# Optimization experiments

Hardware: AMD Instinct MI355X
Metric: run time of the kernel (lower is better)

Reference implementation:

```python
import jax, jax.numpy as jnp
import numpy as np

B, C, N, T, H = 4, 128, 512, 16, 4
DK = C // H
SCALE = float(np.sqrt(DK) * 1.0)  # dk**0.5 * max(tau,1e-6), tau=1.0


def setup_inputs() -> dict:
    key = jax.random.key(0)
    ks = jax.random.split(key, 6)
    x = jax.random.normal(ks[0], (B, C, N, T), jnp.float32)
    Wq = jax.random.normal(ks[1], (C, C), jnp.float32) * (1.0 / np.sqrt(C))
    Wk = jax.random.normal(ks[2], (C, C), jnp.float32) * (1.0 / np.sqrt(C))
    # original init is identity; add tiny noise so it's not degenerate
    structural = jnp.eye(N, dtype=jnp.float32) + 0.01 * jax.random.normal(ks[3], (N, N), jnp.float32)
    fusion_w = jax.random.normal(ks[4], (2,), jnp.float32) * 0.5  # 1x1 conv over 2 input channels
    fusion_b = (jax.random.normal(ks[5], (), jnp.float32) * 0.1)
    return {"x": x, "Wq": Wq, "Wk": Wk, "structural": structural,
            "fusion_w": fusion_w, "fusion_b": fusion_b}


def reference(x, Wq, Wk, structural, fusion_w, fusion_b):
    # x: [B, C, N, T]. 1x1 conv == per-channel linear; arrange to [B,T,N,H,DK]
    Q = jnp.einsum('oc,bcnt->btno', Wq, x).reshape(B, T, N, H, DK)
    K = jnp.einsum('oc,bcnt->btno', Wk, x).reshape(B, T, N, H, DK)
    # scores: [B, T, H, N, N]
    scores = jnp.einsum('btnhd,btmhd->bthnm', Q, K) / SCALE
    att_node = jax.nn.softmax(scores, axis=-1).mean(axis=(1, 2))  # [B, N, N]
    att_struct = jax.nn.softmax(structural, axis=-1)              # [N, N]
    # fusion conv (1x1, 2->1 channels) == weighted sum + bias
    fused = fusion_w[0] * att_node + fusion_w[1] * att_struct[None] + fusion_b
    fused = 0.5 * (fused + jnp.swapaxes(fused, 1, 2))  # symmetrize
    fused = jax.nn.softmax(fused, axis=-1)             # normalize='softmax'
    x_bt = jnp.transpose(x, (0, 3, 2, 1))              # [B, T, N, C]
    x_att = jnp.einsum('bij,btjc->btic', fused, x_bt)  # weighted aggregation over nodes
    return jnp.transpose(x_att, (0, 3, 2, 1))          # [B, C, N, T]
```

## Files before the change

kernel.cpp:

```cpp
#include <hip/hip_runtime.h>

#define BB 4
#define CC 128
#define NN 512
#define TT 16
#define HH 4
#define DKK 32
#define INV_SCALE 0.17677669529663687f

typedef __attribute__((ext_vector_type(8))) short bf16x8;
typedef __attribute__((ext_vector_type(4))) float f32x4;

__device__ __forceinline__ unsigned int pk2bf(float a, float b) {
  unsigned int ua = __float_as_uint(a);
  ua = (ua + 0x7FFFu + ((ua >> 16) & 1u)) >> 16;
  unsigned int ub = __float_as_uint(b);
  ub = (ub + 0x7FFFu + ((ub >> 16) & 1u)) >> 16;
  return ua | (ub << 16);
}

__device__ __forceinline__ ushort cv1(float f) {
  unsigned int u = __float_as_uint(f);
  return (ushort)((u + 0x7FFFu + ((u >> 16) & 1u)) >> 16);
}

__device__ __forceinline__ unsigned int pkfast(float a, float b) {
  unsigned int au = __float_as_uint(a) + 0x8000u;
  unsigned int bu = __float_as_uint(b) + 0x8000u;
  return __builtin_amdgcn_perm(bu, au, 0x07060302u);
}

__global__ __launch_bounds__(256) void k_wconv(const float* __restrict__ Wq,
                                               const float* __restrict__ Wk,
                                               ushort* __restrict__ Wqb,
                                               ushort* __restrict__ Wkb) {
  const int gid = blockIdx.x * 256 + threadIdx.x;
  const int i = gid * 4;
  const float* src = (i < 16384) ? (Wq + i) : (Wk + i - 16384);
  ushort* dst = (i < 16384) ? (Wqb + i) : (Wkb + i - 16384);
  float4 v = *(const float4*)src;
  uint2 u;
  u.x = pk2bf(v.x, v.y);
  u.y = pk2bf(v.z, v.w);
  *(uint2*)dst = u;
}

__global__ __launch_bounds__(256) void k_proj(const float* __restrict__ x,
                                              const ushort* __restrict__ Wqb,
                                              const ushort* __restrict__ Wkb,
                                              ushort* __restrict__ Qb,
                                              ushort* __restrict__ Kb) {
  __shared__ float xl[128 * 128];
  const int b = blockIdx.y;
  const int nt0 = blockIdx.x * 128;
  const int tid = threadIdx.x;
  const int w = tid >> 6, lane = tid & 63;
  const int lm = lane & 15, quad = lane >> 4;

  const float* xb = x + (size_t)b * 1048576 + nt0;
#pragma unroll
  for (int L = tid * 4; L < 16384; L += 1024) {
    int c = L >> 7, j = L & 127;
    *(float4*)(xl + L) = *(const float4*)(xb + c * 8192 + j);
  }

  const int o0 = w * 32;
  bf16x8 aq[2][4], ak[2][4];
#pragma unroll
  for (int ot = 0; ot < 2; ++ot)
#pragma unroll
    for (int kc = 0; kc < 4; ++kc) {
      int off = (o0 + ot * 16 + lm) * 128 + kc * 32 + quad * 8;
      aq[ot][kc] = *(const bf16x8*)(Wqb + off);
      ak[ot][kc] = *(const bf16x8*)(Wkb + off);
    }
  __syncthreads();

  const int nq = nt0 >> 4;
#pragma unroll 2
  for (int jt = 0; jt < 8; ++jt) {
    bf16x8 bfr[4];
#pragma unroll
    for (int kc = 0; kc < 4; ++kc) {
      const float* sp = xl + (kc * 32 + quad * 8) * 128 + jt * 16 + lm;
      float f0 = sp[0],   f1 = sp[128], f2 = sp[256], f3 = sp[384];
      float f4 = sp[512], f5 = sp[640], f6 = sp[768], f7 = sp[896];
      uint4 u;
      u.x = pkfast(f0, f1);
      u.y = pkfast(f2, f3);
      u.z = pkfast(f4, f5);
      u.w = pkfast(f6, f7);
      union { uint4 u; bf16x8 v; } cv;
      cv.u = u;
      bfr[kc] = cv.v;
    }

    f32x4 accq0 = {0,0,0,0}, accq1 = {0,0,0,0};
    f32x4 acck0 = {0,0,0,0}, acck1 = {0,0,0,0};
#pragma unroll
    for (int kc = 0; kc < 4; ++kc) {
      accq0 = __builtin_amdgcn_mfma_f32_16x16x32_bf16(aq[0][kc], bfr[kc], accq0, 0, 0, 0);
      accq1 = __builtin_amdgcn_mfma_f32_16x16x32_bf16(aq[1][kc], bfr[kc], accq1, 0, 0, 0);
      acck0 = __builtin_amdgcn_mfma_f32_16x16x32_bf16(ak[0][kc], bfr[kc], acck0, 0, 0, 0);
      acck1 = __builtin_amdgcn_mfma_f32_16x16x32_bf16(ak[1][kc], bfr[kc], acck1, 0, 0, 0);
    }

    const size_t base = (size_t)b * 1048576 + (size_t)lm * 65536 + w * 16384 +
                        (size_t)(nq + jt) * 32 + quad * 4;
    uint2 uq0, uq1, uk0, uk1;
    uq0.x = pk2bf(accq0[0], accq0[1]); uq0.y = pk2bf(accq0[2], accq0[3]);
    uq1.x = pk2bf(accq1[0], accq1[1]); uq1.y = pk2bf(accq1[2], accq1[3]);
    uk0.x = pk2bf(acck0[0], acck0[1]); uk0.y = pk2bf(acck0[2], acck0[3]);
    uk1.x = pk2bf(acck1[0], acck1[1]); uk1.y = pk2bf(acck1[2], acck1[3]);
    *(uint2*)(Qb + base)      = uq0;
    *(uint2*)(Qb + base + 16) = uq1;
    *(uint2*)(Kb + base)      = uk0;
    *(uint2*)(Kb + base + 16) = uk1;
  }
}

__global__ __launch_bounds__(64) void k_scores(const ushort* __restrict__ Qb,
                                               const ushort* __restrict__ Kb,
                                               ushort* __restrict__ part) {
  __shared__ float SH[16 * 516];
  const int strip = blockIdx.x, g = blockIdx.y, b = blockIdx.z;
  const int lane = threadIdx.x;
  const int lm = lane & 15, quad = lane >> 4;
  const int n0 = strip * 16;
  const int d0 = quad * 8;
  const int r2 = lane >> 2, cb2 = (lane & 3) * 4;
  const int rsel = r2 & 3;

  float acc[128];
#pragma unroll
  for (int i = 0; i < 128; ++i) acc[i] = 0.f;

  for (int pi = 0; pi < 8; ++pi) {
    const int p = (g << 3) + pi, t = p >> 2, h = p & 3;
    const size_t base = (size_t)(((b * 16 + t) * 4 + h)) * 16384;
    bf16x8 afrag = *(const bf16x8*)(Qb + base + (size_t)(n0 + lm) * 32 + d0);
    float rp0 = 0.f, rp1 = 0.f, rp2 = 0.f, rp3 = 0.f;
    bf16x8 bfrag = *(const bf16x8*)(Kb + base + (size_t)lm * 32 + d0);
#pragma unroll 4
    for (int ct = 0; ct < 32; ++ct) {
      bf16x8 curb = bfrag;
      if (ct < 31)
        bfrag = *(const bf16x8*)(Kb + base + (size_t)((ct + 1) * 16 + lm) * 32 + d0);
      f32x4 z = {0.f, 0.f, 0.f, 0.f};
      f32x4 dv = __builtin_amdgcn_mfma_f32_16x16x32_bf16(afrag, curb, z, 0, 0, 0);
      float e0 = __expf(dv[0] * INV_SCALE);
      float e1 = __expf(dv[1] * INV_SCALE);
      float e2 = __expf(dv[2] * INV_SCALE);
      float e3 = __expf(dv[3] * INV_SCALE);
      float* sp = SH + (quad * 4) * 516 + ct * 16 + lm;
      sp[0] = e0; sp[516] = e1; sp[1032] = e2; sp[1548] = e3;
      rp0 += e0; rp1 += e1; rp2 += e2; rp3 += e3;
    }
#pragma unroll
    for (int m = 1; m < 16; m <<= 1) {
      rp0 += __shfl_xor(rp0, m);
      rp1 += __shfl_xor(rp1, m);
      rp2 += __shfl_xor(rp2, m);
      rp3 += __shfl_xor(rp3, m);
    }
    float rs = (rsel == 0) ? rp0 : (rsel == 1) ? rp1 : (rsel == 2) ? rp2 : rp3;
    float inv = 1.0f / rs;
    __builtin_amdgcn_s_waitcnt(0xC07F);
#pragma unroll
    for (int k = 0; k < 32; ++k) {
      f32x4 v = *(const f32x4*)(SH + r2 * 516 + cb2 + k * 16);
      acc[k * 4 + 0] = fmaf(v[0], inv, acc[k * 4 + 0]);
      acc[k * 4 + 1] = fmaf(v[1], inv, acc[k * 4 + 1]);
      acc[k * 4 + 2] = fmaf(v[2], inv, acc[k * 4 + 2]);
      acc[k * 4 + 3] = fmaf(v[3], inv, acc[k * 4 + 3]);
    }
  }

  ushort* po = part + ((size_t)((g * 4 + b) * 512 + n0 + r2)) * 512 + cb2;
#pragma unroll
  for (int k = 0; k < 32; ++k) {
    uint2 u;
    u.x = pk2bf(acc[k * 4 + 0], acc[k * 4 + 1]);
    u.y = pk2bf(acc[k * 4 + 2], acc[k * 4 + 3]);
    *(uint2*)(po + k * 16) = u;
  }
}

__global__ __launch_bounds__(256) void k_reduce(const ushort* __restrict__ part,
                                                float* __restrict__ accA) {
  const int gid = blockIdx.x * 256 + threadIdx.x;
  const size_t idx = (size_t)gid * 4;
  float s0 = 0.f, s1 = 0.f, s2 = 0.f, s3 = 0.f;
#pragma unroll
  for (int g = 0; g < 8; ++g) {
    ushort4 v = *(const ushort4*)(part + (size_t)g * 1048576 + idx);
    s0 += __uint_as_float((unsigned int)v.x << 16);
    s1 += __uint_as_float((unsigned int)v.y << 16);
    s2 += __uint_as_float((unsigned int)v.z << 16);
    s3 += __uint_as_float((unsigned int)v.w << 16);
  }
  float4 o = make_float4(s0, s1, s2, s3);
  *(float4*)(accA + idx) = o;
}

__global__ __launch_bounds__(256) void k_sym(float* __restrict__ accA,
                                             float* __restrict__ st) {
  __shared__ float L1[64 * 68];
  __shared__ float L2[64 * 68];
  const int z = blockIdx.y;
  float* M = (z < 4) ? (accA + (size_t)z * 262144) : st;
  int rem = blockIdx.x, ti = 0;
  for (;;) { int cnt = 8 - ti; if (rem < cnt) break; rem -= cnt; ++ti; }
  const int tj = ti + rem;
  const bool diag = (ti == tj);
  const int tid = threadIdx.x;

#pragma unroll
  for (int it = 0; it < 4; ++it) {
    int L = tid * 4 + it * 1024;
    int r = L >> 6, c = L & 63;
    *(float4*)(L1 + r * 68 + c) = *(const float4*)(M + (ti * 64 + r) * 512 + tj * 64 + c);
    if (!diag)
      *(float4*)(L2 + r * 68 + c) = *(const float4*)(M + (tj * 64 + r) * 512 + ti * 64 + c);
  }
  __syncthreads();

  const float* LT = diag ? L1 : L2;
#pragma unroll
  for (int it = 0; it < 4; ++it) {
    int L = tid * 4 + it * 1024;
    int r = L >> 6, c = L & 63;
    float4 o1;
    o1.x = L1[r * 68 + c + 0] + LT[(c + 0) * 68 + r];
    o1.y = L1[r * 68 + c + 1] + LT[(c + 1) * 68 + r];
    o1.z = L1[r * 68 + c + 2] + LT[(c + 2) * 68 + r];
    o1.w = L1[r * 68 + c + 3] + LT[(c + 3) * 68 + r];
    *(float4*)(M + (ti * 64 + r) * 512 + tj * 64 + c) = o1;
    if (!diag) {
      float4 o2;
      o2.x = L2[r * 68 + c + 0] + L1[(c + 0) * 68 + r];
      o2.y = L2[r * 68 + c + 1] + L1[(c + 1) * 68 + r];
      o2.z = L2[r * 68 + c + 2] + L1[(c + 2) * 68 + r];
      o2.w = L2[r * 68 + c + 3] + L1[(c + 3) * 68 + r];
      *(float4*)(M + (tj * 64 + r) * 512 + ti * 64 + c) = o2;
    }
  }
}

__global__ __launch_bounds__(256) void k_xconv(const float* __restrict__ x,
                                               ushort* __restrict__ xtb) {
  __shared__ ushort xs[16 * 520];
  const int c = blockIdx.x, b = blockIdx.y;
  const int tid = threadIdx.x;
  const float* in = x + ((size_t)b * 128 + c) * 8192;
  ushort* outp = xtb + ((size_t)b * 128 + c) * 8192;

#pragma unroll
  for (int it = 0; it < 8; ++it) {
    int idx = (tid + it * 256) * 4;
    int j = idx >> 4, t0 = idx & 15;
    float4 v = *(const float4*)(in + idx);
    xs[(t0 + 0) * 520 + j] = cv1(v.x);
    xs[(t0 + 1) * 520 + j] = cv1(v.y);
    xs[(t0 + 2) * 520 + j] = cv1(v.z);
    xs[(t0 + 3) * 520 + j] = cv1(v.w);
  }
  __syncthreads();
#pragma unroll
  for (int it = 0; it < 4; ++it) {
    int u = (tid + it * 256) * 8;
    int t = u >> 9, j0 = u & 511;
    *(uint4*)(outp + u) = *(const uint4*)(xs + t * 520 + j0);
  }
}

__device__ __forceinline__ float blk_max(float v, float* red, int tid) {
#pragma unroll
  for (int off = 32; off > 0; off >>= 1) v = fmaxf(v, __shfl_xor(v, off, 64));
  if ((tid & 63) == 0) red[tid >> 6] = v;
  __syncthreads();
  v = fmaxf(fmaxf(red[0], red[1]), fmaxf(red[2], red[3]));
  __syncthreads();
  return v;
}
__device__ __forceinline__ float blk_sum(float v, float* red, int tid) {
#pragma unroll
  for (int off = 32; off > 0; off >>= 1) v += __shfl_xor(v, off, 64);
  if ((tid & 63) == 0) red[tid >> 6] = v;
  __syncthreads();
  v = (red[0] + red[1]) + (red[2] + red[3]);
  __syncthreads();
  return v;
}

__global__ __launch_bounds__(256) void k_struct(const float* __restrict__ S,
                                                float* __restrict__ st) {
  __shared__ float red[4];
  const int i = blockIdx.x, tid = threadIdx.x;
  float s0 = S[i * 512 + tid], s1 = S[i * 512 + tid + 256];
  float m = blk_max(fmaxf(s0, s1), red, tid);
  float e0 = __expf(s0 - m), e1 = __expf(s1 - m);
  float sum = blk_sum(e0 + e1, red, tid);
  float inv = 1.0f / sum;
  st[i * 512 + tid] = e0 * inv;
  st[i * 512 + tid + 256] = e1 * inv;
}

__global__ __launch_bounds__(256) void k_fused(const float* __restrict__ accA,
                                               const float* __restrict__ st,
                                               const float* __restrict__ fw,
                                               const float* __restrict__ fb,
                                               ushort* __restrict__ fusedb) {
  __shared__ float red[4];
  const int i = blockIdx.x, b = blockIdx.y, tid = threadIdx.x;
  const float w0s = fw[0] * (0.5f / 64.f);
  const float w1s = fw[1] * 0.5f;
  const float bias = fb[0];
  const float* A = accA + (size_t)b * 262144 + (size_t)i * 512;
  const float* S = st + (size_t)i * 512;
  float2 a2 = *(const float2*)(A + tid * 2);
  float2 s2 = *(const float2*)(S + tid * 2);
  float l0 = fmaf(w0s, a2.x, fmaf(w1s, s2.x, bias));
  float l1 = fmaf(w0s, a2.y, fmaf(w1s, s2.y, bias));
  float m = blk_max(fmaxf(l0, l1), red, tid);
  float e0 = __expf(l0 - m), e1 = __expf(l1 - m);
  float sum = blk_sum(e0 + e1, red, tid);
  float inv = 1.0f / sum;
  *(unsigned int*)(fusedb + ((size_t)(b * 512 + i)) * 512 + tid * 2) =
      pk2bf(e0 * inv, e1 * inv);
}

__global__ __launch_bounds__(256) void k_agg(const ushort* __restrict__ fusedb,
                                             const ushort* __restrict__ xtb,
                                             float* __restrict__ out) {
  __shared__ ushort xs[16 * 520];
  const int cg = blockIdx.x;
  const int i0 = blockIdx.y * 64;
  const int b = blockIdx.z;
  const int tid = threadIdx.x, w = tid >> 6, lane = tid & 63;
  const int lm = lane & 15, quad = lane >> 4;

  const ushort* fr = fusedb + ((size_t)(b * 512 + i0 + w * 16 + lm)) * 512 + quad * 8;
  bf16x8 af[16];
#pragma unroll
  for (int kk = 0; kk < 16; ++kk) af[kk] = *(const bf16x8*)(fr + kk * 32);

  const ushort* xg = xtb + ((size_t)b * 128 + cg * 8) * 8192;
  uint4 rg[4];
#pragma unroll
  for (int it = 0; it < 4; ++it) rg[it] = *(const uint4*)(xg + (tid + it * 256) * 8);

  for (int c = 0; c < 8; ++c) {
#pragma unroll
    for (int it = 0; it < 4; ++it) {
      int u = (tid + it * 256) * 8;
      int t = u >> 9, j0 = u & 511;
      *(uint4*)(xs + t * 520 + j0) = rg[it];
    }
    __syncthreads();
    if (c < 7) {
      const ushort* xg2 = xg + (size_t)(c + 1) * 8192;
#pragma unroll
      for (int it = 0; it < 4; ++it) rg[it] = *(const uint4*)(xg2 + (tid + it * 256) * 8);
    }
    f32x4 acc = {0.f, 0.f, 0.f, 0.f};
#pragma unroll
    for (int kk = 0; kk < 16; ++kk) {
      bf16x8 bf = *(const bf16x8*)(xs + lm * 520 + kk * 32 + quad * 8);
      acc = __builtin_amdgcn_mfma_f32_16x16x32_bf16(af[kk], bf, acc, 0, 0, 0);
    }
    float* op = out + (size_t)b * 1048576 + (size_t)(cg * 8 + c) * 8192 +
                (size_t)(i0 + w * 16 + quad * 4) * 16 + lm;
    op[0]  = acc[0];
    op[16] = acc[1];
    op[32] = acc[2];
    op[48] = acc[3];
    __syncthreads();
  }
}

extern "C" void kernel_launch(void* const* d_in, const int* in_sizes, int n_in,
                              void* d_out, int out_size, void* d_ws, size_t ws_size,
                              hipStream_t stream) {
  const float* x  = (const float*)d_in[0];
  const float* Wq = (const float*)d_in[1];
  const float* Wk = (const float*)d_in[2];
  const float* S  = (const float*)d_in[3];
  const float* fw = (const float*)d_in[4];
  const float* fb = (const float*)d_in[5];
  float* out = (float*)d_out;

  ushort* Qb   = (ushort*)d_ws;
  ushort* Kb   = Qb + 4194304;
  ushort* part = Kb + 4194304;
  ushort* xtb  = (ushort*)d_ws;
  float* accA  = (float*)d_ws + 8388608;
  float* st    = accA + 1048576;
  ushort* fusedb = (ushort*)(st + 262144);
  ushort* Wqb  = fusedb + 1048576;
  ushort* Wkb  = Wqb + 16384;

  k_wconv <<<dim3(32),        256, 0, stream>>>(Wq, Wk, Wqb, Wkb);
  k_proj  <<<dim3(64, 4),     256, 0, stream>>>(x, Wqb, Wkb, Qb, Kb);
  k_scores<<<dim3(32, 8, 4),   64, 0, stream>>>(Qb, Kb, part);
  k_struct<<<dim3(512),       256, 0, stream>>>(S, st);
  k_reduce<<<dim3(1024),      256, 0, stream>>>(part, accA);
  k_sym   <<<dim3(36, 5),     256, 0, stream>>>(accA, st);
  k_xconv <<<dim3(128, 4),    256, 0, stream>>>(x, xtb);
  k_fused <<<dim3(512, 4),    256, 0, stream>>>(accA, st, fw, fb, fusedb);
  k_agg   <<<dim3(16, 8, 4),  256, 0, stream>>>(fusedb, xtb, out);
}
```

Before: 184.1 us.

## Split score columns across four waves with shared-memory row-sum reduction

k_scores moves from one 64-thread wave per block to four waves, each covering 128 of the 512 key columns. Exponentials stay in registers instead of round-tripping through shared memory. Row sums are combined across waves through a small double-buffered shared array with a barrier per (t,h) pair. The accumulator shrinks from 128 to 32 floats per lane, which raises occupancy and cuts per-wave serial work, at the cost of a __syncthreads each iteration and a final shared-memory transpose for coalesced stores.

```diff
diff --git a/kernel.cpp b/kernel.cpp
--- a/kernel.cpp
+++ b/kernel.cpp
@@ -119,41 +119,48 @@
   }
 }
 
-__global__ __launch_bounds__(64) void k_scores(const ushort* __restrict__ Qb,
-                                               const ushort* __restrict__ Kb,
-                                               ushort* __restrict__ part) {
+__global__ __launch_bounds__(256, 4) void k_scores(const ushort* __restrict__ Qb,
+                                                   const ushort* __restrict__ Kb,
+                                                   ushort* __restrict__ part) {
   __shared__ float SH[16 * 516];
+  __shared__ float red[2][4][16];
   const int strip = blockIdx.x, g = blockIdx.y, b = blockIdx.z;
-  const int lane = threadIdx.x;
+  const int tid = threadIdx.x;
+  const int w = tid >> 6, lane = tid & 63;
   const int lm = lane & 15, quad = lane >> 4;
   const int n0 = strip * 16;
-  const int d0 = quad * 8;
-  const int r2 = lane >> 2, cb2 = (lane & 3) * 4;
-  const int rsel = r2 & 3;
-
-  float acc[128];
-#pragma unroll
-  for (int i = 0; i < 128; ++i) acc[i] = 0.f;
+  const int wcol0 = w * 128;
+
+  float acc[32];
+#pragma unroll
+  for (int i = 0; i < 32; ++i) acc[i] = 0.f;
 
   for (int pi = 0; pi < 8; ++pi) {
-    const int p = (g << 3) + pi, t = p >> 2, h = p & 3;
-    const size_t base = (size_t)(((b * 16 + t) * 4 + h)) * 16384;
-    bf16x8 afrag = *(const bf16x8*)(Qb + base + (size_t)(n0 + lm) * 32 + d0);
+    const int p = (g << 3) + pi;
+    const size_t base = (size_t)((b * 16 + (p >> 2)) * 4 + (p & 3)) * 16384;
+    bf16x8 afrag = *(const bf16x8*)(Qb + base + (size_t)(n0 + lm) * 32 + quad * 8);
+    bf16x8 bfr[8];
+#pragma unroll
+    for (int ct = 0; ct < 8; ++ct)
+      bfr[ct] = *(const bf16x8*)(Kb + base + (size_t)(wcol0 + ct * 16 + lm) * 32 + quad * 8);
+
+    f32x4 d[8];
+#pragma unroll
+    for (int ct = 0; ct < 8; ++ct) {
+      f32x4 z = {0.f, 0.f, 0.f, 0.f};
+      d[ct] = __builtin_amdgcn_mfma_f32_16x16x32_bf16(afrag, bfr[ct], z, 0, 0, 0);
+    }
+
+    float cur[32];
     float rp0 = 0.f, rp1 = 0.f, rp2 = 0.f, rp3 = 0.f;
-    bf16x8 bfrag = *(const bf16x8*)(Kb + base + (size_t)lm * 32 + d0);
-#pragma unroll 4
-    for (int ct = 0; ct < 32; ++ct) {
-      bf16x8 curb = bfrag;
-      if (ct < 31)
-        bfrag = *(const bf16x8*)(Kb + base + (size_t)((ct + 1) * 16 + lm) * 32 + d0);
-      f32x4 z = {0.f, 0.f, 0.f, 0.f};
-      f32x4 dv = __builtin_amdgcn_mfma_f32_16x16x32_bf16(afrag, curb, z, 0, 0, 0);
-      float e0 = __expf(dv[0] * INV_SCALE);
-      float e1 = __expf(dv[1] * INV_SCALE);
-      float e2 = __expf(dv[2] * INV_SCALE);
-      float e3 = __expf(dv[3] * INV_SCALE);
-      float* sp = SH + (quad * 4) * 516 + ct * 16 + lm;
-      sp[0] = e0; sp[516] = e1; sp[1032] = e2; sp[1548] = e3;
+#pragma unroll
+    for (int ct = 0; ct < 8; ++ct) {
+      float e0 = __expf(d[ct][0] * INV_SCALE);
+      float e1 = __expf(d[ct][1] * INV_SCALE);
+      float e2 = __expf(d[ct][2] * INV_SCALE);
+      float e3 = __expf(d[ct][3] * INV_SCALE);
+      cur[ct * 4 + 0] = e0; cur[ct * 4 + 1] = e1;
+      cur[ct * 4 + 2] = e2; cur[ct * 4 + 3] = e3;
       rp0 += e0; rp1 += e1; rp2 += e2; rp3 += e3;
     }
 #pragma unroll
@@ -163,26 +170,40 @@
       rp2 += __shfl_xor(rp2, m);
       rp3 += __shfl_xor(rp3, m);
     }
-    float rs = (rsel == 0) ? rp0 : (rsel == 1) ? rp1 : (rsel == 2) ? rp2 : rp3;
-    float inv = 1.0f / rs;
-    __builtin_amdgcn_s_waitcnt(0xC07F);
-#pragma unroll
-    for (int k = 0; k < 32; ++k) {
-      f32x4 v = *(const f32x4*)(SH + r2 * 516 + cb2 + k * 16);
-      acc[k * 4 + 0] = fmaf(v[0], inv, acc[k * 4 + 0]);
-      acc[k * 4 + 1] = fmaf(v[1], inv, acc[k * 4 + 1]);
-      acc[k * 4 + 2] = fmaf(v[2], inv, acc[k * 4 + 2]);
-      acc[k * 4 + 3] = fmaf(v[3], inv, acc[k * 4 + 3]);
-    }
-  }
-
-  ushort* po = part + ((size_t)((g * 4 + b) * 512 + n0 + r2)) * 512 + cb2;
-#pragma unroll
-  for (int k = 0; k < 32; ++k) {
+    if (lm == 0) {
+      red[pi & 1][w][quad * 4 + 0] = rp0;
+      red[pi & 1][w][quad * 4 + 1] = rp1;
+      red[pi & 1][w][quad * 4 + 2] = rp2;
+      red[pi & 1][w][quad * 4 + 3] = rp3;
+    }
+    __syncthreads();
+#pragma unroll
+    for (int r = 0; r < 4; ++r) {
+      float rs = red[pi & 1][0][quad * 4 + r] + red[pi & 1][1][quad * 4 + r] +
+                 red[pi & 1][2][quad * 4 + r] + red[pi & 1][3][quad * 4 + r];
+      float inv = 1.0f / rs;
+#pragma unroll
+      for (int ct = 0; ct < 8; ++ct)
+        acc[ct * 4 + r] = fmaf(cur[ct * 4 + r], inv, acc[ct * 4 + r]);
+    }
+  }
+
+#pragma unroll
+  for (int ct = 0; ct < 8; ++ct) {
+#pragma unroll
+    for (int r = 0; r < 4; ++r)
+      SH[(quad * 4 + r) * 516 + wcol0 + ct * 16 + lm] = acc[ct * 4 + r];
+  }
+  __syncthreads();
+  const int row = tid >> 4, colb = (tid & 15) * 4;
+  ushort* po = part + ((size_t)((g * 4 + b) * 512 + n0 + row)) * 512 + colb;
+#pragma unroll
+  for (int k = 0; k < 8; ++k) {
+    f32x4 v = *(const f32x4*)(SH + row * 516 + colb + k * 64);
     uint2 u;
-    u.x = pk2bf(acc[k * 4 + 0], acc[k * 4 + 1]);
-    u.y = pk2bf(acc[k * 4 + 2], acc[k * 4 + 3]);
-    *(uint2*)(po + k * 16) = u;
+    u.x = pk2bf(v[0], v[1]);
+    u.y = pk2bf(v[2], v[3]);
+    *(uint2*)(po + k * 64) = u;
   }
 }
 
@@ -402,7 +423,7 @@
 
   k_wconv <<<dim3(32),        256, 0, stream>>>(Wq, Wk, Wqb, Wkb);
   k_proj  <<<dim3(64, 4),     256, 0, stream>>>(x, Wqb, Wkb, Qb, Kb);
-  k_scores<<<dim3(32, 8, 4),   64, 0, stream>>>(Qb, Kb, part);
+  k_scores<<<dim3(32, 8, 4),  256, 0, stream>>>(Qb, Kb, part);
   k_struct<<<dim3(512),       256, 0, stream>>>(S, st);
   k_reduce<<<dim3(1024),      256, 0, stream>>>(part, accA);
   k_sym   <<<dim3(36, 5),     256, 0, stream>>>(accA, st);
```

After: 162.2 us. -11.9%, faster.
